# Performance work log

Hardware: AMD Instinct MI355X
Metric: run time of the kernel (lower is better)

Reference implementation:

```python
import jax, jax.numpy as jnp
import numpy as np

D_MODEL = 1024
NUM_HEADS = 16
D_K = D_MODEL // NUM_HEADS
SIM_THRESH = 0.7


def setup_inputs() -> dict:
    key = jax.random.key(0)
    ks = jax.random.split(key, 7)
    bs, seq = 2, 2048
    scale = 1.0 / np.sqrt(D_MODEL)
    x = jax.random.normal(ks[0], (bs, seq, D_MODEL), dtype=jnp.float32)
    Wq = jax.random.normal(ks[1], (D_MODEL, D_MODEL), dtype=jnp.float32) * scale
    Wk = jax.random.normal(ks[2], (D_MODEL, D_MODEL), dtype=jnp.float32) * scale
    Wv = jax.random.normal(ks[3], (D_MODEL, D_MODEL), dtype=jnp.float32) * scale
    bq = jax.random.normal(ks[4], (D_MODEL,), dtype=jnp.float32) * scale
    bk = jax.random.normal(ks[5], (D_MODEL,), dtype=jnp.float32) * scale
    bv = jax.random.normal(ks[6], (D_MODEL,), dtype=jnp.float32) * scale
    return {"x": x, "Wq": Wq, "bq": bq, "Wk": Wk, "bk": bk, "Wv": Wv, "bv": bv}


def reference(x, Wq, bq, Wk, bk, Wv, bv):
    bs, seq, d_model = x.shape
    # dynamic structural mask: cosine similarity > 0.7, shared across heads
    norm_x = x / jnp.maximum(jnp.linalg.norm(x, axis=-1, keepdims=True), 1e-12)
    sim = jnp.einsum('bsd,btd->bst', norm_x, norm_x)          # [B,S,S]
    mask = (sim > SIM_THRESH)[:, None, :, :]                  # [B,1,S,S]

    def proj(W, b):
        y = x @ W.T + b                                        # [B,S,D]
        return y.reshape(bs, seq, NUM_HEADS, D_K).transpose(0, 2, 1, 3)  # [B,H,S,dk]

    q = proj(Wq, bq)
    k = proj(Wk, bk)
    v = proj(Wv, bv)

    scores = jnp.einsum('bhsd,bhtd->bhst', q, k) / jnp.sqrt(jnp.float32(D_K))
    scores = jnp.where(mask, scores, -jnp.inf)
    attn = jax.nn.softmax(scores, axis=-1)                     # diag always unmasked
    return jnp.einsum('bhst,bhtd->bhsd', attn, v)              # [B,H,S,dk]
```

## Files before the change

kernel.cpp:

```cpp
#include <hip/hip_runtime.h>
#include <stdint.h>
#include <math.h>

#define D_MODEL 1024
#define NUM_HEADS 16
#define D_K 64
#define SEQ 2048
#define BATCH 2
#define SIM_THRESH 0.7f
#define ITHRESH 11290

#define TS 128
#define BKV 32
#define NITV (D_MODEL / BKV)
#define BKS 64
#define NITS (D_MODEL / BKS)

#define NROWS (BATCH * SEQ)
#define VP_BLOCKS ((NROWS / TS) * (D_MODEL / TS))
#define SIM_ROWB (SEQ / TS)
#define SIM_TRI (SIM_ROWB * (SIM_ROWB + 1) / 2)
#define SIM_BLOCKS (SIM_TRI * BATCH)
#define GRID (VP_BLOCKS + SIM_BLOCKS)
#define VP_PER_XCD (VP_BLOCKS / 8)
#define SIM_PER_XCD (SIM_BLOCKS / 8)

#define TILE_B 8192

typedef __attribute__((ext_vector_type(8))) short bf16x8;
typedef __attribute__((ext_vector_type(4))) float f32x4;
typedef __attribute__((ext_vector_type(4))) int i32x4;

static __device__ __forceinline__ unsigned short f2bf(float f) {
    unsigned int u = __float_as_uint(f);
    unsigned int r = (u + 0x7FFF + ((u >> 16) & 1)) >> 16;
    return (unsigned short)r;
}
static __device__ __forceinline__ float bf2f(unsigned short u) {
    return __uint_as_float(((unsigned int)u) << 16);
}

__global__ __launch_bounds__(256) void k_prep(const float* __restrict__ x,
                                              const float* __restrict__ Wv,
                                              unsigned short* __restrict__ xn,
                                              unsigned short* __restrict__ Wvb,
                                              char* __restrict__ xq,
                                              float* __restrict__ norms,
                                              int* __restrict__ cnt) {
    int bid = blockIdx.x, tid = threadIdx.x;
    if (bid < NROWS) {
        const float4* xr = (const float4*)(x + (size_t)bid * D_MODEL);
        float4 vv = xr[tid];
        float ss = vv.x * vv.x + vv.y * vv.y + vv.z * vv.z + vv.w * vv.w;
        for (int off = 32; off > 0; off >>= 1) ss += __shfl_down(ss, off, 64);
        __shared__ float wsum[4];
        int lane = tid & 63, wv = tid >> 6;
        if (lane == 0) wsum[wv] = ss;
        __syncthreads();
        float nrm = sqrtf(wsum[0] + wsum[1] + wsum[2] + wsum[3]);
        float inv = 1.0f / fmaxf(nrm, 1e-12f);
        float n0 = vv.x * inv, n1 = vv.y * inv, n2 = vv.z * inv, n3 = vv.w * inv;
        ushort4 o;
        o.x = f2bf(n0); o.y = f2bf(n1); o.z = f2bf(n2); o.w = f2bf(n3);
        *(ushort4*)(xn + (size_t)bid * D_MODEL + tid * 4) = o;
        char4 q;
        q.x = (char)__float2int_rn(n0 * 127.f);
        q.y = (char)__float2int_rn(n1 * 127.f);
        q.z = (char)__float2int_rn(n2 * 127.f);
        q.w = (char)__float2int_rn(n3 * 127.f);
        *(char4*)(xq + (size_t)bid * D_MODEL + tid * 4) = q;
        if (tid == 0) { norms[bid] = nrm; cnt[bid] = 0; }
    } else {
        size_t i = (size_t)(bid - NROWS) * 256 + tid;
        float4 w = ((const float4*)Wv)[i];
        ushort4 o;
        o.x = f2bf(w.x); o.y = f2bf(w.y); o.z = f2bf(w.z); o.w = f2bf(w.w);
        *(ushort4*)(Wvb + i * 4) = o;
    }
}

static __device__ __forceinline__ void stage8k(const char* __restrict__ gsrc,
                                               int rowStrideB, int kByte,
                                               char* ldsDst, int tid) {
#pragma unroll
    for (int i = 0; i < 2; ++i) {
        int c   = i * 256 + tid;
        int row = c >> 2;
        int ch  = c & 3;
        const char* ga = gsrc + (size_t)row * rowStrideB + kByte + ch * 16;
        __builtin_amdgcn_global_load_lds(
            (const __attribute__((address_space(1))) unsigned int*)ga,
            (__attribute__((address_space(3))) unsigned int*)(ldsDst + c * 16),
            16, 0, 0);
    }
}

__global__ __launch_bounds__(256, 3) void k_main(const unsigned short* __restrict__ xn,
                                                 const unsigned short* __restrict__ Wvb,
                                                 const char* __restrict__ xq,
                                                 const float* __restrict__ bv,
                                                 const float* __restrict__ norms,
                                                 int* __restrict__ cnt,
                                                 float* __restrict__ out) {
    __shared__ char As[2 * TILE_B];
    __shared__ char Bs[2 * TILE_B];
    int bid0 = blockIdx.x;
    int xcd = bid0 & 7, l = bid0 >> 3;
    int tid = threadIdx.x;
    int lane = tid & 63, wave = tid >> 6;
    int wm = wave & 1, wn = wave >> 1;
    int lrow = lane & 15, quad = lane >> 4;

    bool isV = (l < VP_PER_XCD);

    int aoffB[4], boffB[4];
#pragma unroll
    for (int i = 0; i < 4; ++i) {
        aoffB[i] = (wm * 64 + i * 16 + lrow) * 64 + quad * 16;
        boffB[i] = (wn * 64 + i * 16 + lrow) * 64 + quad * 16;
    }

    if (isV) {
        int bid = xcd * VP_PER_XCD + l;
        int rowBase = (bid >> 3) * TS;
        int colBase = (bid & 7) * TS;
        const char* Asrc = (const char*)(xn + (size_t)rowBase * D_MODEL);
        const char* Bsrc = (const char*)(Wvb + (size_t)colBase * D_MODEL);

        f32x4 acc[4][4] = {};
        stage8k(Asrc, D_MODEL * 2, 0, As, tid);
        stage8k(Bsrc, D_MODEL * 2, 0, Bs, tid);
        __syncthreads();
        for (int it = 0; it < NITV; ++it) {
            int cur = it & 1, nxt = cur ^ 1;
            if (it + 1 < NITV) {
                stage8k(Asrc, D_MODEL * 2, (it + 1) * 64, As + nxt * TILE_B, tid);
                stage8k(Bsrc, D_MODEL * 2, (it + 1) * 64, Bs + nxt * TILE_B, tid);
            }
            const char* Ac = As + cur * TILE_B;
            const char* Bc = Bs + cur * TILE_B;
            bf16x8 av[4], bw[4];
#pragma unroll
            for (int i = 0; i < 4; ++i) av[i] = *(const bf16x8*)(Ac + aoffB[i]);
#pragma unroll
            for (int i = 0; i < 4; ++i) bw[i] = *(const bf16x8*)(Bc + boffB[i]);
#pragma unroll
            for (int mt = 0; mt < 4; ++mt)
#pragma unroll
                for (int nt = 0; nt < 4; ++nt)
                    acc[mt][nt] = __builtin_amdgcn_mfma_f32_16x16x32_bf16(av[mt], bw[nt], acc[mt][nt], 0, 0, 0);
            __syncthreads();
        }
#pragma unroll
        for (int nt = 0; nt < 4; ++nt) {
            int n = colBase + wn * 64 + nt * 16 + lrow;
            float bn = bv[n];
            int h = n >> 6, j = n & 63;
#pragma unroll
            for (int mt = 0; mt < 4; ++mt) {
#pragma unroll
                for (int r = 0; r < 4; ++r) {
                    int m = rowBase + wm * 64 + mt * 16 + quad * 4 + r;
                    float val = acc[mt][nt][r] * norms[m] + bn;
                    int bb = m >> 11, s = m & (SEQ - 1);
                    out[(((size_t)(bb * NUM_HEADS + h)) * SEQ + s) * D_K + j] = val;
                }
            }
        }
    } else {
        int sidx = xcd * SIM_PER_XCD + (l - VP_PER_XCD);
        int b = (sidx >= SIM_TRI) ? 1 : 0;
        int r0 = sidx - b * SIM_TRI;
        int bi = 0;
        while (r0 >= SIM_ROWB - bi) { r0 -= SIM_ROWB - bi; ++bi; }
        int bj = bi + r0;
        int rowBase = bi * TS;
        int colBase = bj * TS;
        const char* base = xq + (size_t)b * SEQ * D_MODEL;
        const char* Asrc = base + (size_t)rowBase * D_MODEL;
        const char* Bsrc = base + (size_t)colBase * D_MODEL;

        i32x4 acc[4][4] = {};
        stage8k(Asrc, D_MODEL, 0, As, tid);
        stage8k(Bsrc, D_MODEL, 0, Bs, tid);
        __syncthreads();
        for (int it = 0; it < NITS; ++it) {
            int cur = it & 1, nxt = cur ^ 1;
            if (it + 1 < NITS) {
                stage8k(Asrc, D_MODEL, (it + 1) * 64, As + nxt * TILE_B, tid);
                stage8k(Bsrc, D_MODEL, (it + 1) * 64, Bs + nxt * TILE_B, tid);
            }
            const char* Ac = As + cur * TILE_B;
            const char* Bc = Bs + cur * TILE_B;
            i32x4 av[4], bw[4];
#pragma unroll
            for (int i = 0; i < 4; ++i) av[i] = *(const i32x4*)(Ac + aoffB[i]);
#pragma unroll
            for (int i = 0; i < 4; ++i) bw[i] = *(const i32x4*)(Bc + boffB[i]);
#pragma unroll
            for (int mt = 0; mt < 4; ++mt)
#pragma unroll
                for (int nt = 0; nt < 4; ++nt)
                    acc[mt][nt] = __builtin_amdgcn_mfma_i32_16x16x64_i8(av[mt], bw[nt], acc[mt][nt], 0, 0, 0);
            __syncthreads();
        }
        int* cb = cnt + b * SEQ;
        bool diag = (bi == bj);
#pragma unroll
        for (int nt = 0; nt < 4; ++nt) {
            int n = colBase + wn * 64 + nt * 16 + lrow;
#pragma unroll
            for (int mt = 0; mt < 4; ++mt) {
#pragma unroll
                for (int r = 0; r < 4; ++r) {
                    int m = rowBase + wm * 64 + mt * 16 + quad * 4 + r;
                    if (acc[mt][nt][r] > ITHRESH) {
                        atomicAdd(&cb[m], 1);
                        if (!diag) atomicAdd(&cb[n], 1);
                    }
                }
            }
        }
    }
}

__global__ __launch_bounds__(256) void k_fix(
    const float* __restrict__ x,
    const float* __restrict__ Wq, const float* __restrict__ bq,
    const float* __restrict__ Wk, const float* __restrict__ bk,
    const float* __restrict__ Wv, const float* __restrict__ bv,
    const unsigned short* __restrict__ xn,
    const int* __restrict__ cnt,
    float* __restrict__ out)
{
    int tid = threadIdx.x;
    int rowBase = blockIdx.x * 256;

    __shared__ int list[256];
    __shared__ int nlist;
    if (tid == 0) nlist = 0;
    __syncthreads();
    int grow = rowBase + tid;
    if (cnt[grow] != 1) { int p = atomicAdd(&nlist, 1); list[p] = grow; }
    __syncthreads();
    int nfix = nlist;
    if (nfix == 0) return;

    __shared__ uint8_t mrow[SEQ];
    __shared__ float q_row[D_MODEL];
    __shared__ float k_row[D_MODEL];
    __shared__ float v_row[D_MODEL];
    __shared__ float accO[D_MODEL];
    __shared__ float m_h[NUM_HEADS], l_h[NUM_HEADS], alpha_h[NUM_HEADS], p_h[NUM_HEADS];

    for (int li = 0; li < nfix; ++li) {
        int row = list[li];
        int b = row >> 11, s = row & (SEQ - 1);

        const unsigned short* xs = xn + (size_t)row * D_MODEL;
        for (int t = tid; t < SEQ; t += 256) {
            const unsigned short* xt = xn + ((size_t)b * SEQ + t) * D_MODEL;
            float d = 0.f;
            for (int k = 0; k < D_MODEL; ++k) d += bf2f(xs[k]) * bf2f(xt[k]);
            mrow[t] = (d > SIM_THRESH) ? 1 : 0;
        }

        const float* xrow = x + (size_t)row * D_MODEL;
        for (int c = tid; c < D_MODEL; c += 256) {
            const float* w = Wq + (size_t)c * D_MODEL;
            float acc = bq[c];
            for (int d = 0; d < D_MODEL; ++d) acc += xrow[d] * w[d];
            q_row[c] = acc;
            accO[c] = 0.f;
        }
        if (tid < NUM_HEADS) { m_h[tid] = -INFINITY; l_h[tid] = 0.f; }
        __syncthreads();

        for (int t = 0; t < SEQ; ++t) {
            if (!mrow[t]) continue;
            const float* xt = x + ((size_t)b * SEQ + t) * D_MODEL;
            for (int c = tid; c < D_MODEL; c += 256) {
                const float* wk = Wk + (size_t)c * D_MODEL;
                const float* wv = Wv + (size_t)c * D_MODEL;
                float ak = bk[c], av = bv[c];
                for (int d = 0; d < D_MODEL; ++d) {
                    float xv = xt[d];
                    ak += xv * wk[d];
                    av += xv * wv[d];
                }
                k_row[c] = ak;
                v_row[c] = av;
            }
            __syncthreads();
            if (tid < NUM_HEADS) {
                float sc = 0.f;
                for (int j = 0; j < D_K; ++j) sc += q_row[tid * D_K + j] * k_row[tid * D_K + j];
                sc *= 0.125f;
                float mnew = fmaxf(m_h[tid], sc);
                float alpha = expf(m_h[tid] - mnew);
                float p = expf(sc - mnew);
                l_h[tid] = l_h[tid] * alpha + p;
                m_h[tid] = mnew;
                alpha_h[tid] = alpha;
                p_h[tid] = p;
            }
            __syncthreads();
            for (int c = tid; c < D_MODEL; c += 256) {
                int h = c >> 6;
                accO[c] = accO[c] * alpha_h[h] + p_h[h] * v_row[c];
            }
            __syncthreads();
        }
        for (int c = tid; c < D_MODEL; c += 256) {
            int h = c >> 6, j = c & 63;
            out[(((size_t)(b * NUM_HEADS + h)) * SEQ + s) * D_K + j] = accO[c] / l_h[h];
        }
        __syncthreads();
    }
}

extern "C" void kernel_launch(void* const* d_in, const int* in_sizes, int n_in,
                              void* d_out, int out_size, void* d_ws, size_t ws_size,
                              hipStream_t stream) {
    const float* x  = (const float*)d_in[0];
    const float* Wq = (const float*)d_in[1];
    const float* bq = (const float*)d_in[2];
    const float* Wk = (const float*)d_in[3];
    const float* bk = (const float*)d_in[4];
    const float* Wv = (const float*)d_in[5];
    const float* bv = (const float*)d_in[6];
    float* out = (float*)d_out;

    unsigned short* xn  = (unsigned short*)d_ws;
    unsigned short* Wvb = xn + (size_t)NROWS * D_MODEL;
    char* xq     = (char*)(Wvb + (size_t)D_MODEL * D_MODEL);
    float* norms = (float*)(xq + (size_t)NROWS * D_MODEL);
    int* cnt     = (int*)(norms + NROWS);

    k_prep<<<NROWS + D_MODEL * D_MODEL / 1024, 256, 0, stream>>>(x, Wv, xn, Wvb, xq, norms, cnt);

    k_main<<<GRID, 256, 0, stream>>>(xn, Wvb, xq, bv, norms, cnt, out);

    k_fix<<<NROWS / 256, 256, 0, stream>>>(x, Wq, bq, Wk, bk, Wv, bv, xn, cnt, out);
}
```

Before: 109.4 us.

## Deepen LDS pipeline to four stages and skip redundant B loads on diagonal tiles

Both GEMM paths now use a four-slot LDS ring and process two K-steps per barrier, halving the number of __syncthreads calls and prefetching two stages ahead. For diagonal similarity tiles, the B operand is read from the A buffer instead of being loaded a second time. LDS use doubles to 64KB per block and launch bounds drop from 3 to 2 blocks per CU, trading occupancy for fewer barriers and deeper prefetch.

```diff
diff --git a/kernel.cpp b/kernel.cpp
--- a/kernel.cpp
+++ b/kernel.cpp
@@ -11,10 +11,8 @@
 #define ITHRESH 11290
 
 #define TS 128
-#define BKV 32
-#define NITV (D_MODEL / BKV)
-#define BKS 64
-#define NITS (D_MODEL / BKS)
+#define NITV (D_MODEL / 32)
+#define NITS (D_MODEL / 64)
 
 #define NROWS (BATCH * SEQ)
 #define VP_BLOCKS ((NROWS / TS) * (D_MODEL / TS))
@@ -95,15 +93,15 @@
     }
 }
 
-__global__ __launch_bounds__(256, 3) void k_main(const unsigned short* __restrict__ xn,
+__global__ __launch_bounds__(256, 2) void k_main(const unsigned short* __restrict__ xn,
                                                  const unsigned short* __restrict__ Wvb,
                                                  const char* __restrict__ xq,
                                                  const float* __restrict__ bv,
                                                  const float* __restrict__ norms,
                                                  int* __restrict__ cnt,
                                                  float* __restrict__ out) {
-    __shared__ char As[2 * TILE_B];
-    __shared__ char Bs[2 * TILE_B];
+    __shared__ char As[4 * TILE_B];
+    __shared__ char Bs[4 * TILE_B];
     int bid0 = blockIdx.x;
     int xcd = bid0 & 7, l = bid0 >> 3;
     int tid = threadIdx.x;
@@ -128,27 +126,34 @@
         const char* Bsrc = (const char*)(Wvb + (size_t)colBase * D_MODEL);
 
         f32x4 acc[4][4] = {};
-        stage8k(Asrc, D_MODEL * 2, 0, As, tid);
-        stage8k(Bsrc, D_MODEL * 2, 0, Bs, tid);
-        __syncthreads();
-        for (int it = 0; it < NITV; ++it) {
-            int cur = it & 1, nxt = cur ^ 1;
-            if (it + 1 < NITV) {
-                stage8k(Asrc, D_MODEL * 2, (it + 1) * 64, As + nxt * TILE_B, tid);
-                stage8k(Bsrc, D_MODEL * 2, (it + 1) * 64, Bs + nxt * TILE_B, tid);
-            }
-            const char* Ac = As + cur * TILE_B;
-            const char* Bc = Bs + cur * TILE_B;
-            bf16x8 av[4], bw[4];
-#pragma unroll
-            for (int i = 0; i < 4; ++i) av[i] = *(const bf16x8*)(Ac + aoffB[i]);
-#pragma unroll
-            for (int i = 0; i < 4; ++i) bw[i] = *(const bf16x8*)(Bc + boffB[i]);
-#pragma unroll
-            for (int mt = 0; mt < 4; ++mt)
-#pragma unroll
-                for (int nt = 0; nt < 4; ++nt)
-                    acc[mt][nt] = __builtin_amdgcn_mfma_f32_16x16x32_bf16(av[mt], bw[nt], acc[mt][nt], 0, 0, 0);
+        stage8k(Asrc, 2048, 0, As, tid);
+        stage8k(Bsrc, 2048, 0, Bs, tid);
+        stage8k(Asrc, 2048, 64, As + TILE_B, tid);
+        stage8k(Bsrc, 2048, 64, Bs + TILE_B, tid);
+        __syncthreads();
+        for (int t = 0; t < NITV / 2; ++t) {
+            if (t + 1 < NITV / 2) {
+                int s0 = (2 * t + 2) & 3, s1 = (2 * t + 3) & 3;
+                stage8k(Asrc, 2048, (2 * t + 2) * 64, As + s0 * TILE_B, tid);
+                stage8k(Bsrc, 2048, (2 * t + 2) * 64, Bs + s0 * TILE_B, tid);
+                stage8k(Asrc, 2048, (2 * t + 3) * 64, As + s1 * TILE_B, tid);
+                stage8k(Bsrc, 2048, (2 * t + 3) * 64, Bs + s1 * TILE_B, tid);
+            }
+#pragma unroll
+            for (int sub = 0; sub < 2; ++sub) {
+                const char* Ac = As + ((2 * t + sub) & 3) * TILE_B;
+                const char* Bc = Bs + ((2 * t + sub) & 3) * TILE_B;
+                bf16x8 av[4], bw[4];
+#pragma unroll
+                for (int i = 0; i < 4; ++i) av[i] = *(const bf16x8*)(Ac + aoffB[i]);
+#pragma unroll
+                for (int i = 0; i < 4; ++i) bw[i] = *(const bf16x8*)(Bc + boffB[i]);
+#pragma unroll
+                for (int mt = 0; mt < 4; ++mt)
+#pragma unroll
+                    for (int nt = 0; nt < 4; ++nt)
+                        acc[mt][nt] = __builtin_amdgcn_mfma_f32_16x16x32_bf16(av[mt], bw[nt], acc[mt][nt], 0, 0, 0);
+            }
             __syncthreads();
         }
 #pragma unroll
@@ -179,33 +184,44 @@
         const char* base = xq + (size_t)b * SEQ * D_MODEL;
         const char* Asrc = base + (size_t)rowBase * D_MODEL;
         const char* Bsrc = base + (size_t)colBase * D_MODEL;
+        bool diag = (bi == bj);
 
         i32x4 acc[4][4] = {};
-        stage8k(Asrc, D_MODEL, 0, As, tid);
-        stage8k(Bsrc, D_MODEL, 0, Bs, tid);
-        __syncthreads();
-        for (int it = 0; it < NITS; ++it) {
-            int cur = it & 1, nxt = cur ^ 1;
-            if (it + 1 < NITS) {
-                stage8k(Asrc, D_MODEL, (it + 1) * 64, As + nxt * TILE_B, tid);
-                stage8k(Bsrc, D_MODEL, (it + 1) * 64, Bs + nxt * TILE_B, tid);
-            }
-            const char* Ac = As + cur * TILE_B;
-            const char* Bc = Bs + cur * TILE_B;
-            i32x4 av[4], bw[4];
-#pragma unroll
-            for (int i = 0; i < 4; ++i) av[i] = *(const i32x4*)(Ac + aoffB[i]);
-#pragma unroll
-            for (int i = 0; i < 4; ++i) bw[i] = *(const i32x4*)(Bc + boffB[i]);
-#pragma unroll
-            for (int mt = 0; mt < 4; ++mt)
-#pragma unroll
-                for (int nt = 0; nt < 4; ++nt)
-                    acc[mt][nt] = __builtin_amdgcn_mfma_i32_16x16x64_i8(av[mt], bw[nt], acc[mt][nt], 0, 0, 0);
+        stage8k(Asrc, 1024, 0, As, tid);
+        stage8k(Asrc, 1024, 64, As + TILE_B, tid);
+        if (!diag) {
+            stage8k(Bsrc, 1024, 0, Bs, tid);
+            stage8k(Bsrc, 1024, 64, Bs + TILE_B, tid);
+        }
+        __syncthreads();
+        for (int t = 0; t < NITS / 2; ++t) {
+            if (t + 1 < NITS / 2) {
+                int s0 = (2 * t + 2) & 3, s1 = (2 * t + 3) & 3;
+                stage8k(Asrc, 1024, (2 * t + 2) * 64, As + s0 * TILE_B, tid);
+                stage8k(Asrc, 1024, (2 * t + 3) * 64, As + s1 * TILE_B, tid);
+                if (!diag) {
+                    stage8k(Bsrc, 1024, (2 * t + 2) * 64, Bs + s0 * TILE_B, tid);
+                    stage8k(Bsrc, 1024, (2 * t + 3) * 64, Bs + s1 * TILE_B, tid);
+                }
+            }
+#pragma unroll
+            for (int sub = 0; sub < 2; ++sub) {
+                const char* Ac = As + ((2 * t + sub) & 3) * TILE_B;
+                const char* Bc = (diag ? As : Bs) + ((2 * t + sub) & 3) * TILE_B;
+                i32x4 av[4], bw[4];
+#pragma unroll
+                for (int i = 0; i < 4; ++i) av[i] = *(const i32x4*)(Ac + aoffB[i]);
+#pragma unroll
+                for (int i = 0; i < 4; ++i) bw[i] = *(const i32x4*)(Bc + boffB[i]);
+#pragma unroll
+                for (int mt = 0; mt < 4; ++mt)
+#pragma unroll
+                    for (int nt = 0; nt < 4; ++nt)
+                        acc[mt][nt] = __builtin_amdgcn_mfma_i32_16x16x64_i8(av[mt], bw[nt], acc[mt][nt], 0, 0, 0);
+            }
             __syncthreads();
         }
         int* cb = cnt + b * SEQ;
-        bool diag = (bi == bj);
 #pragma unroll
         for (int nt = 0; nt < 4; ++nt) {
             int n = colBase + wn * 64 + nt * 16 + lrow;
```

New measurement: 112.0 us. 2.4% more time.
